# Kernel optimization log

Measured on AMD Instinct MI355X. Metric: run time of the kernel, lower is better.

Reference implementation:

```python
import jax, jax.numpy as jnp
import numpy as np

N0, N1, N2 = 262144, 65536, 16384   # sampled src nodes, layer-1 targets, layer-2 targets
E1, E2 = 1048576, 262144            # fanout 16 edges per layer
IN_C, HID_C, OUT_C = 128, 256, 64


def sage_conv(x_src, x_dst, src, dst, num_dst, W_l, W_r, b):
    # PyG SAGEConv (mean aggr): out = mean_{j in N(i)} x_src[j] @ W_l^T + b + x_dst @ W_r^T
    msgs = x_src[src]                                   # [E, C] gather
    s = jax.ops.segment_sum(msgs, dst, num_segments=num_dst)
    cnt = jax.ops.segment_sum(jnp.ones((src.shape[0],), x_src.dtype), dst,
                              num_segments=num_dst)
    aggr = s / jnp.maximum(cnt, 1.0)[:, None]           # mean; isolated nodes -> 0
    return aggr @ W_l.T + b + x_dst @ W_r.T


def setup_inputs() -> dict:
    key = jax.random.key(0)
    ks = jax.random.split(key, 9)
    inp = {
        "x": jax.random.normal(ks[0], (N0, IN_C), dtype=jnp.float32),
        "src1": jax.random.randint(ks[1], (E1,), 0, N0, dtype=jnp.int32),
        "dst1": jax.random.randint(ks[2], (E1,), 0, N1, dtype=jnp.int32),
        "src2": jax.random.randint(ks[3], (E2,), 0, N1, dtype=jnp.int32),
        "dst2": jax.random.randint(ks[4], (E2,), 0, N2, dtype=jnp.int32),
        "W1_l": jax.random.normal(ks[5], (HID_C, IN_C), dtype=jnp.float32) * 0.05,
        "W1_r": jax.random.normal(ks[6], (HID_C, IN_C), dtype=jnp.float32) * 0.05,
        "b1": jnp.zeros((HID_C,), dtype=jnp.float32),
        "W2_l": jax.random.normal(ks[7], (OUT_C, HID_C), dtype=jnp.float32) * 0.05,
        "W2_r": jax.random.normal(ks[8], (OUT_C, HID_C), dtype=jnp.float32) * 0.05,
        "b2": jnp.zeros((OUT_C,), dtype=jnp.float32),
    }
    return inp


def reference(x, src1, dst1, src2, dst2, W1_l, W1_r, b1, W2_l, W2_r, b2):
    # layer 1: sources = all N0 nodes, targets = first N1 nodes (x_target = x[:size[1]])
    h = sage_conv(x, x[:N1], src1, dst1, N1, W1_l, W1_r, b1)   # [N1, HID_C]
    h = jax.nn.relu(h)   # dropout is identity in eval mode
    # layer 2: sources = N1 layer-1 outputs, targets = first N2
    h = sage_conv(h, h[:N2], src2, dst2, N2, W2_l, W2_r, b2)   # [N2, OUT_C]
    return jax.nn.log_softmax(h, axis=-1)
```

## Files before the change

kernel.cpp:

```cpp
#include <hip/hip_runtime.h>
#include <cstdint>
#include <cstddef>

#define N0C 262144
#define N1C 65536
#define N2C 16384
#define E1C 1048576
#define E2C 262144
#define XN4 (N0C * 128 / 4)
#define XHALF (XN4 / 2)

typedef __attribute__((ext_vector_type(8))) short bf16x8;
typedef __attribute__((ext_vector_type(4))) float f32x4;

__device__ __forceinline__ unsigned short f2bf(float f) {
  union { float f; unsigned u; } q; q.f = f;
  unsigned r = q.u + 0x7fffu + ((q.u >> 16) & 1u);
  return (unsigned short)(r >> 16);
}
__device__ __forceinline__ float blo(unsigned u) {
  union { unsigned u; float f; } q; q.u = u << 16; return q.f;
}
__device__ __forceinline__ float bhi(unsigned u) {
  union { unsigned u; float f; } q; q.u = u & 0xffff0000u; return q.f;
}
__device__ __forceinline__ void gl_lds16(const void* g, void* l) {
  __builtin_amdgcn_global_load_lds((const __attribute__((address_space(1))) void*)g,
                                   (__attribute__((address_space(3))) void*)l, 16, 0, 0);
}

__device__ __forceinline__ void cvt_range(const float4* __restrict__ x,
                                          ushort4* __restrict__ xb,
                                          int i, int stride, int end) {
  for (; i < end; i += stride) {
    float4 v = x[i];
    ushort4 o;
    o.x = f2bf(v.x); o.y = f2bf(v.y); o.z = f2bf(v.z); o.w = f2bf(v.w);
    xb[i] = o;
  }
}

__global__ __launch_bounds__(256) void cvtw_kernel(
    const float4* __restrict__ W1l, const float4* __restrict__ W1r,
    const float4* __restrict__ W2l, const float4* __restrict__ W2r,
    ushort4* __restrict__ W1lb, ushort4* __restrict__ W1rb,
    ushort4* __restrict__ W2lb, ushort4* __restrict__ W2rb,
    int* __restrict__ btail) {
  int y = blockIdx.y;
  int i = blockIdx.x * 256 + threadIdx.x;
  if (y == 4) {
    if (i < 512) btail[i] = 0;
    return;
  }
  const float4* in; ushort4* outp; int n4;
  if (y == 0)      { in = W1l; outp = W1lb; n4 = 8192; }
  else if (y == 1) { in = W1r; outp = W1rb; n4 = 8192; }
  else if (y == 2) { in = W2l; outp = W2lb; n4 = 4096; }
  else             { in = W2r; outp = W2rb; n4 = 4096; }
  if (i < n4) {
    float4 v = in[i];
    ushort4 o;
    o.x = f2bf(v.x); o.y = f2bf(v.y); o.z = f2bf(v.z); o.w = f2bf(v.w);
    outp[i] = o;
  }
}

__global__ __launch_bounds__(256) void mega_kernel(
    const int* __restrict__ src1, const int* __restrict__ dst1,
    const int* __restrict__ src2, const int* __restrict__ dst2,
    int* __restrict__ btail, unsigned* __restrict__ pair1, unsigned* __restrict__ pair2,
    const float4* __restrict__ x, ushort4* __restrict__ xb) {
  __shared__ int hist[256];
  __shared__ int lofs[256];
  __shared__ int gbase[256];
  __shared__ unsigned stg[4096];
  __shared__ unsigned char bstg[4096];
  int b = blockIdx.x;
  int t = threadIdx.x;
  if (b >= 320) {
    cvt_range(x, xb, (b - 320) * 256 + t, 2048 * 256, XHALF);
    return;
  }
  const int* src; const int* dst; int shift; int dmask; int* bt; unsigned* pb; int e0;
  if (b < 256) { src = src1; dst = dst1; shift = 8; dmask = 255; bt = btail;       pb = pair1; e0 = b * 4096; }
  else         { src = src2; dst = dst2; shift = 6; dmask = 63;  bt = btail + 256; pb = pair2; e0 = (b - 256) * 4096; }
  hist[t] = 0;
  __syncthreads();
  unsigned pk[16]; int bk[16], rk[16];
#pragma unroll
  for (int k = 0; k < 16; ++k) {
    int e = e0 + k * 256 + t;
    int s = src[e];
    int d = dst[e];
    bk[k] = d >> shift;
    pk[k] = ((unsigned)(d & dmask) << 18) | (unsigned)s;
    rk[k] = atomicAdd(&hist[bk[k]], 1);
  }
  __syncthreads();
  int v = hist[t];
  lofs[t] = v;
  __syncthreads();
  for (int ofs = 1; ofs < 256; ofs <<= 1) {
    int add = (t >= ofs) ? lofs[t - ofs] : 0;
    __syncthreads();
    lofs[t] += add;
    __syncthreads();
  }
  gbase[t] = atomicAdd(&bt[t], v);
  int excl = lofs[t] - v;
  lofs[t] = excl;
  __syncthreads();
#pragma unroll
  for (int k = 0; k < 16; ++k) {
    int p = lofs[bk[k]] + rk[k];
    stg[p] = pk[k];
    bstg[p] = (unsigned char)bk[k];
  }
  __syncthreads();
  for (int i = t; i < 4096; i += 256) {
    int bki = bstg[i];
    int idx = gbase[bki] + (i - lofs[bki]);
    if (idx < 8192)
      pb[(size_t)bki * 8192 + idx] = stg[i];
  }
}

__global__ __launch_bounds__(256) void binB_kernel(
    const unsigned* __restrict__ pair1, const unsigned* __restrict__ pair2,
    const int* __restrict__ btail,
    int* __restrict__ off1, int* __restrict__ cnt1, int* __restrict__ ssrc1,
    int* __restrict__ off2, int* __restrict__ cnt2, int* __restrict__ ssrc2,
    const float4* __restrict__ x, ushort4* __restrict__ xb) {
  __shared__ int lcnt[256];
  __shared__ int loff[256];
  __shared__ int lcnt2[256];
  __shared__ unsigned stage[8192];
  int b = blockIdx.x;
  int t = threadIdx.x;
  if (b >= 512) {
    cvt_range(x, xb, XHALF + (b - 512) * 256 + t, 2048 * 256, XN4);
    return;
  }
  const unsigned* pb; const int* bt; int dpb; int* off; int* cnt; int* ssrc; int bl;
  if (b < 256) { bl = b;       pb = pair1 + (size_t)bl * 8192; bt = btail;       dpb = 256; off = off1; cnt = cnt1; ssrc = ssrc1; }
  else         { bl = b - 256; pb = pair2 + (size_t)bl * 8192; bt = btail + 256; dpb = 64;  off = off2; cnt = cnt2; ssrc = ssrc2; }
  lcnt[t] = (t < bl) ? bt[t] : 0;
  __syncthreads();
  for (int ofs = 128; ofs > 0; ofs >>= 1) {
    if (t < ofs) lcnt[t] += lcnt[t + ofs];
    __syncthreads();
  }
  int base = lcnt[0];
  __syncthreads();
  lcnt[t] = 0;
  lcnt2[t] = 0;
  __syncthreads();
  int n = bt[bl];
  if (n > 8192) n = 8192;
  for (int i = t; i < n; i += 256) {
    unsigned p = pb[i];
    atomicAdd(&lcnt[p >> 18], 1);
  }
  __syncthreads();
  int v = lcnt[t];
  loff[t] = v;
  __syncthreads();
  for (int ofs = 1; ofs < 256; ofs <<= 1) {
    int add = (t >= ofs) ? loff[t - ofs] : 0;
    __syncthreads();
    loff[t] += add;
    __syncthreads();
  }
  int excl = loff[t] - v;
  loff[t] = excl;
  if (t < dpb) {
    cnt[bl * dpb + t] = v;
    off[bl * dpb + t] = base + excl;
  }
  __syncthreads();
  for (int i = t; i < n; i += 256) {
    unsigned p = pb[i];
    int dl = p >> 18;
    int r = atomicAdd(&lcnt2[dl], 1);
    stage[loff[dl] + r] = p & 0x3FFFFu;
  }
  __syncthreads();
  for (int i = t; i < n; i += 256) ssrc[base + i] = (int)stage[i];
}

__global__ __launch_bounds__(256) void agg1_kernel(const ushort* __restrict__ xb,
                                                   const int* __restrict__ ssrc,
                                                   const int* __restrict__ off,
                                                   const int* __restrict__ cnt,
                                                   ushort* __restrict__ aggr) {
  int wid = (blockIdx.x * 256 + threadIdx.x) >> 6;
  int lane = threadIdx.x & 63;
  int grp = lane >> 4;
  int cl = lane & 15;
  int start = __builtin_amdgcn_readfirstlane(off[wid]);
  int n = __builtin_amdgcn_readfirstlane(cnt[wid]);
  float a0 = 0.f, a1 = 0.f, a2 = 0.f, a3 = 0.f, a4 = 0.f, a5 = 0.f, a6 = 0.f, a7 = 0.f;
  int j = 0;
  for (; j + 8 <= n; j += 8) {
    int sa = ssrc[start + j + grp];
    int sb = ssrc[start + j + 4 + grp];
    uint4 va = *(const uint4*)(xb + (size_t)sa * 128 + cl * 8);
    uint4 vb = *(const uint4*)(xb + (size_t)sb * 128 + cl * 8);
    a0 += blo(va.x) + blo(vb.x); a1 += bhi(va.x) + bhi(vb.x);
    a2 += blo(va.y) + blo(vb.y); a3 += bhi(va.y) + bhi(vb.y);
    a4 += blo(va.z) + blo(vb.z); a5 += bhi(va.z) + bhi(vb.z);
    a6 += blo(va.w) + blo(vb.w); a7 += bhi(va.w) + bhi(vb.w);
  }
  if (j + 4 <= n) {
    int s = ssrc[start + j + grp];
    uint4 v = *(const uint4*)(xb + (size_t)s * 128 + cl * 8);
    a0 += blo(v.x); a1 += bhi(v.x); a2 += blo(v.y); a3 += bhi(v.y);
    a4 += blo(v.z); a5 += bhi(v.z); a6 += blo(v.w); a7 += bhi(v.w);
    j += 4;
  }
  if (grp < n - j) {
    int s = ssrc[start + j + grp];
    uint4 v = *(const uint4*)(xb + (size_t)s * 128 + cl * 8);
    a0 += blo(v.x); a1 += bhi(v.x); a2 += blo(v.y); a3 += bhi(v.y);
    a4 += blo(v.z); a5 += bhi(v.z); a6 += blo(v.w); a7 += bhi(v.w);
  }
#define RED1(v) v += __shfl_xor(v, 16); v += __shfl_xor(v, 32);
  RED1(a0) RED1(a1) RED1(a2) RED1(a3) RED1(a4) RED1(a5) RED1(a6) RED1(a7)
#undef RED1
  if (lane < 16) {
    float inv = (n > 0) ? 1.0f / (float)n : 0.f;
    uint4 o;
    o.x = (unsigned)f2bf(a0 * inv) | ((unsigned)f2bf(a1 * inv) << 16);
    o.y = (unsigned)f2bf(a2 * inv) | ((unsigned)f2bf(a3 * inv) << 16);
    o.z = (unsigned)f2bf(a4 * inv) | ((unsigned)f2bf(a5 * inv) << 16);
    o.w = (unsigned)f2bf(a6 * inv) | ((unsigned)f2bf(a7 * inv) << 16);
    *(uint4*)(aggr + (size_t)wid * 128 + cl * 8) = o;
  }
}

__global__ __launch_bounds__(256) void agg2_kernel(const ushort* __restrict__ h1b,
                                                   const int* __restrict__ ssrc,
                                                   const int* __restrict__ off,
                                                   const int* __restrict__ cnt,
                                                   ushort* __restrict__ aggr) {
  int wid = (blockIdx.x * 256 + threadIdx.x) >> 6;
  int lane = threadIdx.x & 63;
  int grp = lane >> 5;
  int cl = lane & 31;
  int start = __builtin_amdgcn_readfirstlane(off[wid]);
  int n = __builtin_amdgcn_readfirstlane(cnt[wid]);
  float a0 = 0.f, a1 = 0.f, a2 = 0.f, a3 = 0.f, a4 = 0.f, a5 = 0.f, a6 = 0.f, a7 = 0.f;
  int j = 0;
  for (; j + 8 <= n; j += 8) {
    int s0 = ssrc[start + j + grp];
    int s1 = ssrc[start + j + 2 + grp];
    int s2 = ssrc[start + j + 4 + grp];
    int s3 = ssrc[start + j + 6 + grp];
    uint4 v0 = *(const uint4*)(h1b + (size_t)s0 * 256 + cl * 8);
    uint4 v1 = *(const uint4*)(h1b + (size_t)s1 * 256 + cl * 8);
    uint4 v2 = *(const uint4*)(h1b + (size_t)s2 * 256 + cl * 8);
    uint4 v3 = *(const uint4*)(h1b + (size_t)s3 * 256 + cl * 8);
    a0 += blo(v0.x) + blo(v1.x) + blo(v2.x) + blo(v3.x);
    a1 += bhi(v0.x) + bhi(v1.x) + bhi(v2.x) + bhi(v3.x);
    a2 += blo(v0.y) + blo(v1.y) + blo(v2.y) + blo(v3.y);
    a3 += bhi(v0.y) + bhi(v1.y) + bhi(v2.y) + bhi(v3.y);
    a4 += blo(v0.z) + blo(v1.z) + blo(v2.z) + blo(v3.z);
    a5 += bhi(v0.z) + bhi(v1.z) + bhi(v2.z) + bhi(v3.z);
    a6 += blo(v0.w) + blo(v1.w) + blo(v2.w) + blo(v3.w);
    a7 += bhi(v0.w) + bhi(v1.w) + bhi(v2.w) + bhi(v3.w);
  }
  for (; j + 2 <= n; j += 2) {
    int s = ssrc[start + j + grp];
    uint4 v = *(const uint4*)(h1b + (size_t)s * 256 + cl * 8);
    a0 += blo(v.x); a1 += bhi(v.x); a2 += blo(v.y); a3 += bhi(v.y);
    a4 += blo(v.z); a5 += bhi(v.z); a6 += blo(v.w); a7 += bhi(v.w);
  }
  if (grp < n - j) {
    int s = ssrc[start + j + grp];
    uint4 v = *(const uint4*)(h1b + (size_t)s * 256 + cl * 8);
    a0 += blo(v.x); a1 += bhi(v.x); a2 += blo(v.y); a3 += bhi(v.y);
    a4 += blo(v.z); a5 += bhi(v.z); a6 += blo(v.w); a7 += bhi(v.w);
  }
#define RED2(v) v += __shfl_xor(v, 32);
  RED2(a0) RED2(a1) RED2(a2) RED2(a3) RED2(a4) RED2(a5) RED2(a6) RED2(a7)
#undef RED2
  if (lane < 32) {
    float inv = (n > 0) ? 1.0f / (float)n : 0.f;
    uint4 o;
    o.x = (unsigned)f2bf(a0 * inv) | ((unsigned)f2bf(a1 * inv) << 16);
    o.y = (unsigned)f2bf(a2 * inv) | ((unsigned)f2bf(a3 * inv) << 16);
    o.z = (unsigned)f2bf(a4 * inv) | ((unsigned)f2bf(a5 * inv) << 16);
    o.w = (unsigned)f2bf(a6 * inv) | ((unsigned)f2bf(a7 * inv) << 16);
    *(uint4*)(aggr + (size_t)wid * 256 + cl * 8) = o;
  }
}

__global__ __launch_bounds__(512) void mgemm1_kernel(
    const ushort* __restrict__ aggr1, const ushort* __restrict__ xb,
    const ushort* __restrict__ W1lb, const ushort* __restrict__ W1rb,
    const float* __restrict__ b1, ushort* __restrict__ h1b) {
  __shared__ ushort smem[24576];
  ushort* sA = smem;
  ushort* sB = smem + 8192;
  int t = threadIdx.x;
  int lane = t & 63;
  int w = t >> 6;
  int wm = w >> 2, wn = w & 3;
  int i0 = blockIdx.x * 128;

  int sr = t >> 3;
  int sc = (t & 7) ^ (sr & 7);
  int quad = lane >> 4;
  int l15 = lane & 15;
  int xorv = lane & 7;

  f32x4 acc[4][4];
#pragma unroll
  for (int i = 0; i < 4; ++i)
#pragma unroll
    for (int j = 0; j < 4; ++j) acc[i][j] = (f32x4)(0.f);

  for (int kt = 0; kt < 4; ++kt) {
    const ushort* Asrc = (kt < 2) ? aggr1 : xb;
    const ushort* Bsrc = (kt < 2) ? W1lb : W1rb;
    int koff = (kt & 1) * 64;
#pragma unroll
    for (int it = 0; it < 2; ++it) {
      int r = it * 64 + sr;
      gl_lds16(Asrc + (size_t)(i0 + r) * 128 + koff + sc * 8, sA + (it * 512 + t) * 8);
    }
#pragma unroll
    for (int it = 0; it < 4; ++it) {
      int r = it * 64 + sr;
      gl_lds16(Bsrc + (size_t)r * 128 + koff + sc * 8, sB + (it * 512 + t) * 8);
    }
    __syncthreads();
#pragma unroll
    for (int s = 0; s < 2; ++s) {
      int chunk = ((s * 4 + quad) ^ xorv) * 8;
      bf16x8 av[4], bv[4];
#pragma unroll
      for (int fi = 0; fi < 4; ++fi)
        av[fi] = *(const bf16x8*)(sA + (wm * 64 + fi * 16 + l15) * 64 + chunk);
#pragma unroll
      for (int fj = 0; fj < 4; ++fj)
        bv[fj] = *(const bf16x8*)(sB + (wn * 64 + fj * 16 + l15) * 64 + chunk);
#pragma unroll
      for (int fi = 0; fi < 4; ++fi)
#pragma unroll
        for (int fj = 0; fj < 4; ++fj)
          acc[fi][fj] = __builtin_amdgcn_mfma_f32_16x16x32_bf16(av[fi], bv[fj], acc[fi][fj], 0, 0, 0);
    }
    __syncthreads();
  }

  for (int ph = 0; ph < 2; ++ph) {
    if (wm == ph) {
      ushort* eb = smem + (w & 3) * 4096;
#pragma unroll
      for (int fj = 0; fj < 4; ++fj) {
        float bias = b1[wn * 64 + fj * 16 + l15];
#pragma unroll
        for (int fi = 0; fi < 4; ++fi)
#pragma unroll
          for (int r = 0; r < 4; ++r) {
            float v = fmaxf(acc[fi][fj][r] + bias, 0.f);
            eb[(fi * 16 + quad * 4 + r) * 64 + fj * 16 + l15] = f2bf(v);
          }
      }
#pragma unroll
      for (int i = 0; i < 16; ++i) {
        int row = i * 4 + (lane >> 4);
        uint2 v = *(const uint2*)(eb + row * 64 + l15 * 4);
        *(uint2*)(h1b + (size_t)(i0 + wm * 64 + row) * 256 + wn * 64 + l15 * 4) = v;
      }
    }
    __syncthreads();
  }
}

__global__ __launch_bounds__(256) void mgemm2_kernel(
    const ushort* __restrict__ aggr2, const ushort* __restrict__ h1b,
    const ushort* __restrict__ W2lb, const ushort* __restrict__ W2rb,
    const float* __restrict__ b2, float* __restrict__ out) {
  __shared__ ushort sA[64 * 64];
  __shared__ ushort sB[64 * 64];
  int t = threadIdx.x;
  int lane = t & 63;
  int w = t >> 6;
  int i0 = blockIdx.x * 64;

  int sr = t >> 3;
  int sc = (t & 7) ^ (sr & 7);
  int quad = lane >> 4;
  int l15 = lane & 15;
  int xorv = lane & 7;

  f32x4 acc[4];
#pragma unroll
  for (int j = 0; j < 4; ++j) acc[j] = (f32x4)(0.f);

  for (int kt = 0; kt < 8; ++kt) {
    const ushort* Asrc = (kt < 4) ? aggr2 : h1b;
    const ushort* Bsrc = (kt < 4) ? W2lb : W2rb;
    int koff = (kt & 3) * 64;
#pragma unroll
    for (int it = 0; it < 2; ++it) {
      int r = it * 32 + sr;
      gl_lds16(Asrc + (size_t)(i0 + r) * 256 + koff + sc * 8, sA + (it * 256 + t) * 8);
    }
#pragma unroll
    for (int it = 0; it < 2; ++it) {
      int r = it * 32 + sr;
      gl_lds16(Bsrc + (size_t)r * 256 + koff + sc * 8, sB + (it * 256 + t) * 8);
    }
    __syncthreads();
#pragma unroll
    for (int s = 0; s < 2; ++s) {
      int chunk = ((s * 4 + quad) ^ xorv) * 8;
      bf16x8 av = *(const bf16x8*)(sA + (w * 16 + l15) * 64 + chunk);
      bf16x8 bv[4];
#pragma unroll
      for (int fj = 0; fj < 4; ++fj)
        bv[fj] = *(const bf16x8*)(sB + (fj * 16 + l15) * 64 + chunk);
#pragma unroll
      for (int fj = 0; fj < 4; ++fj)
        acc[fj] = __builtin_amdgcn_mfma_f32_16x16x32_bf16(av, bv[fj], acc[fj], 0, 0, 0);
    }
    __syncthreads();
  }

  float b2c[4];
#pragma unroll
  for (int fj = 0; fj < 4; ++fj) b2c[fj] = b2[fj * 16 + l15];

#pragma unroll
  for (int r = 0; r < 4; ++r) {
    int row = i0 + w * 16 + quad * 4 + r;
    float v[4];
#pragma unroll
    for (int fj = 0; fj < 4; ++fj) v[fj] = acc[fj][r] + b2c[fj];
    float m = fmaxf(fmaxf(v[0], v[1]), fmaxf(v[2], v[3]));
    m = fmaxf(m, __shfl_xor(m, 1));
    m = fmaxf(m, __shfl_xor(m, 2));
    m = fmaxf(m, __shfl_xor(m, 4));
    m = fmaxf(m, __shfl_xor(m, 8));
    float ssum = __expf(v[0] - m) + __expf(v[1] - m) + __expf(v[2] - m) + __expf(v[3] - m);
    ssum += __shfl_xor(ssum, 1);
    ssum += __shfl_xor(ssum, 2);
    ssum += __shfl_xor(ssum, 4);
    ssum += __shfl_xor(ssum, 8);
    float lg = m + __logf(ssum);
#pragma unroll
    for (int fj = 0; fj < 4; ++fj)
      out[(size_t)row * 64 + fj * 16 + l15] = v[fj] - lg;
  }
}


extern "C" void kernel_launch(void* const* d_in, const int* in_sizes, int n_in,
                              void* d_out, int out_size, void* d_ws, size_t ws_size,
                              hipStream_t stream) {
  const float* x   = (const float*)d_in[0];
  const int* src1  = (const int*)d_in[1];
  const int* dst1  = (const int*)d_in[2];
  const int* src2  = (const int*)d_in[3];
  const int* dst2  = (const int*)d_in[4];
  const float* W1l = (const float*)d_in[5];
  const float* W1r = (const float*)d_in[6];
  const float* b1  = (const float*)d_in[7];
  const float* W2l = (const float*)d_in[8];
  const float* W2r = (const float*)d_in[9];
  const float* b2  = (const float*)d_in[10];
  float* out = (float*)d_out;

  char* base = (char*)d_ws;
  ushort* xb   = (ushort*)base;
  ushort* ag1b = (ushort*)(base + 67108864);
  ushort* ag2b = (ushort*)(base + 83886080);
  unsigned* pair1 = (unsigned*)(base + 92274688);
  unsigned* pair2 = (unsigned*)(base + 100663296);
  ushort* h1b  = (ushort*)(base + 109051904);
  int* cnt1  = (int*)(base + 142606336);
  int* off1  = cnt1 + N1C;
  int* cnt2  = off1 + N1C;
  int* off2  = cnt2 + N2C;
  int* btail = off2 + N2C;
  int* ssrc1 = btail + 512;
  int* ssrc2 = ssrc1 + E1C;
  ushort* W1lb = (ushort*)(ssrc2 + E2C);
  ushort* W1rb = W1lb + 32768;
  ushort* W2lb = W1rb + 32768;
  ushort* W2rb = W2lb + 16384;

  cvtw_kernel<<<dim3(32, 5), 256, 0, stream>>>(
      (const float4*)W1l, (const float4*)W1r, (const float4*)W2l, (const float4*)W2r,
      (ushort4*)W1lb, (ushort4*)W1rb, (ushort4*)W2lb, (ushort4*)W2rb, btail);

  mega_kernel<<<2368, 256, 0, stream>>>(src1, dst1, src2, dst2, btail, pair1, pair2,
                                        (const float4*)x, (ushort4*)xb);

  binB_kernel<<<2560, 256, 0, stream>>>(pair1, pair2, btail,
                                        off1, cnt1, ssrc1, off2, cnt2, ssrc2,
                                        (const float4*)x, (ushort4*)xb);

  agg1_kernel<<<N1C / 4, 256, 0, stream>>>(xb, ssrc1, off1, cnt1, ag1b);
  mgemm1_kernel<<<N1C / 128, 512, 0, stream>>>(ag1b, xb, W1lb, W1rb, b1, h1b);

  agg2_kernel<<<N2C / 4, 256, 0, stream>>>(h1b, ssrc2, off2, cnt2, ag2b);
  mgemm2_kernel<<<N2C / 64, 256, 0, stream>>>(ag2b, h1b, W2lb, W2rb, b2, out);
}
```

Before: 154.6 us.

## Split layer-1 aggregation and GEMM in halves to overlap them

Layer-1 aggregation and GEMM are split into two row halves. A combined kernel runs the GEMM on the first 32768 rows while its other blocks aggregate the second half, and a final GEMM kernel handles the second half. The aim is to overlap the compute-bound GEMM with the memory-bound gather so the GPU has less idle time between phases. It adds a kernel launch, and because the combined kernel uses 512-thread blocks with a large shared-memory allocation, the aggregation blocks may get lower occupancy.

```diff
diff --git a/kernel.cpp b/kernel.cpp
--- a/kernel.cpp
+++ b/kernel.cpp
@@ -37,6 +37,136 @@
     ushort4 o;
     o.x = f2bf(v.x); o.y = f2bf(v.y); o.z = f2bf(v.z); o.w = f2bf(v.w);
     xb[i] = o;
+  }
+}
+
+__device__ __forceinline__ void agg1_row(const ushort* __restrict__ xb,
+                                         const int* __restrict__ ssrc,
+                                         const int* __restrict__ off,
+                                         const int* __restrict__ cnt,
+                                         ushort* __restrict__ aggr,
+                                         int wid, int lane) {
+  int grp = lane >> 4;
+  int cl = lane & 15;
+  int start = __builtin_amdgcn_readfirstlane(off[wid]);
+  int n = __builtin_amdgcn_readfirstlane(cnt[wid]);
+  float a0 = 0.f, a1 = 0.f, a2 = 0.f, a3 = 0.f, a4 = 0.f, a5 = 0.f, a6 = 0.f, a7 = 0.f;
+  int j = 0;
+  for (; j + 8 <= n; j += 8) {
+    int sa = ssrc[start + j + grp];
+    int sb = ssrc[start + j + 4 + grp];
+    uint4 va = *(const uint4*)(xb + (size_t)sa * 128 + cl * 8);
+    uint4 vb = *(const uint4*)(xb + (size_t)sb * 128 + cl * 8);
+    a0 += blo(va.x) + blo(vb.x); a1 += bhi(va.x) + bhi(vb.x);
+    a2 += blo(va.y) + blo(vb.y); a3 += bhi(va.y) + bhi(vb.y);
+    a4 += blo(va.z) + blo(vb.z); a5 += bhi(va.z) + bhi(vb.z);
+    a6 += blo(va.w) + blo(vb.w); a7 += bhi(va.w) + bhi(vb.w);
+  }
+  if (j + 4 <= n) {
+    int s = ssrc[start + j + grp];
+    uint4 v = *(const uint4*)(xb + (size_t)s * 128 + cl * 8);
+    a0 += blo(v.x); a1 += bhi(v.x); a2 += blo(v.y); a3 += bhi(v.y);
+    a4 += blo(v.z); a5 += bhi(v.z); a6 += blo(v.w); a7 += bhi(v.w);
+    j += 4;
+  }
+  if (grp < n - j) {
+    int s = ssrc[start + j + grp];
+    uint4 v = *(const uint4*)(xb + (size_t)s * 128 + cl * 8);
+    a0 += blo(v.x); a1 += bhi(v.x); a2 += blo(v.y); a3 += bhi(v.y);
+    a4 += blo(v.z); a5 += bhi(v.z); a6 += blo(v.w); a7 += bhi(v.w);
+  }
+#define RED1(v) v += __shfl_xor(v, 16); v += __shfl_xor(v, 32);
+  RED1(a0) RED1(a1) RED1(a2) RED1(a3) RED1(a4) RED1(a5) RED1(a6) RED1(a7)
+#undef RED1
+  if (lane < 16) {
+    float inv = (n > 0) ? 1.0f / (float)n : 0.f;
+    uint4 o;
+    o.x = (unsigned)f2bf(a0 * inv) | ((unsigned)f2bf(a1 * inv) << 16);
+    o.y = (unsigned)f2bf(a2 * inv) | ((unsigned)f2bf(a3 * inv) << 16);
+    o.z = (unsigned)f2bf(a4 * inv) | ((unsigned)f2bf(a5 * inv) << 16);
+    o.w = (unsigned)f2bf(a6 * inv) | ((unsigned)f2bf(a7 * inv) << 16);
+    *(uint4*)(aggr + (size_t)wid * 128 + cl * 8) = o;
+  }
+}
+
+__device__ __forceinline__ void mgemm1_body(
+    const ushort* __restrict__ aggr1, const ushort* __restrict__ xb,
+    const ushort* __restrict__ W1lb, const ushort* __restrict__ W1rb,
+    const float* __restrict__ b1, ushort* __restrict__ h1b,
+    ushort* smem, int i0, int t) {
+  ushort* sA = smem;
+  ushort* sB = smem + 8192;
+  int lane = t & 63;
+  int w = t >> 6;
+  int wm = w >> 2, wn = w & 3;
+  int sr = t >> 3;
+  int sc = (t & 7) ^ (sr & 7);
+  int quad = lane >> 4;
+  int l15 = lane & 15;
+  int xorv = lane & 7;
+
+  f32x4 acc[4][4];
+#pragma unroll
+  for (int i = 0; i < 4; ++i)
+#pragma unroll
+    for (int j = 0; j < 4; ++j) acc[i][j] = (f32x4)(0.f);
+
+  for (int kt = 0; kt < 4; ++kt) {
+    const ushort* Asrc = (kt < 2) ? aggr1 : xb;
+    const ushort* Bsrc = (kt < 2) ? W1lb : W1rb;
+    int koff = (kt & 1) * 64;
+#pragma unroll
+    for (int it = 0; it < 2; ++it) {
+      int r = it * 64 + sr;
+      gl_lds16(Asrc + (size_t)(i0 + r) * 128 + koff + sc * 8, sA + (it * 512 + t) * 8);
+    }
+#pragma unroll
+    for (int it = 0; it < 4; ++it) {
+      int r = it * 64 + sr;
+      gl_lds16(Bsrc + (size_t)r * 128 + koff + sc * 8, sB + (it * 512 + t) * 8);
+    }
+    __syncthreads();
+#pragma unroll
+    for (int s = 0; s < 2; ++s) {
+      int chunk = ((s * 4 + quad) ^ xorv) * 8;
+      bf16x8 av[4], bv[4];
+#pragma unroll
+      for (int fi = 0; fi < 4; ++fi)
+        av[fi] = *(const bf16x8*)(sA + (wm * 64 + fi * 16 + l15) * 64 + chunk);
+#pragma unroll
+      for (int fj = 0; fj < 4; ++fj)
+        bv[fj] = *(const bf16x8*)(sB + (wn * 64 + fj * 16 + l15) * 64 + chunk);
+#pragma unroll
+      for (int fi = 0; fi < 4; ++fi)
+#pragma unroll
+        for (int fj = 0; fj < 4; ++fj)
+          acc[fi][fj] = __builtin_amdgcn_mfma_f32_16x16x32_bf16(av[fi], bv[fj], acc[fi][fj], 0, 0, 0);
+    }
+    __syncthreads();
+  }
+
+  for (int ph = 0; ph < 2; ++ph) {
+    if (wm == ph) {
+      ushort* eb = smem + (w & 3) * 4096;
+#pragma unroll
+      for (int fj = 0; fj < 4; ++fj) {
+        float bias = b1[wn * 64 + fj * 16 + l15];
+#pragma unroll
+        for (int fi = 0; fi < 4; ++fi)
+#pragma unroll
+          for (int r = 0; r < 4; ++r) {
+            float v = fmaxf(acc[fi][fj][r] + bias, 0.f);
+            eb[(fi * 16 + quad * 4 + r) * 64 + fj * 16 + l15] = f2bf(v);
+          }
+      }
+#pragma unroll
+      for (int i = 0; i < 16; ++i) {
+        int row = i * 4 + (lane >> 4);
+        uint2 v = *(const uint2*)(eb + row * 64 + l15 * 4);
+        *(uint2*)(h1b + (size_t)(i0 + wm * 64 + row) * 256 + wn * 64 + l15 * 4) = v;
+      }
+    }
+    __syncthreads();
   }
 }
 
@@ -192,50 +322,35 @@
                                                    const int* __restrict__ ssrc,
                                                    const int* __restrict__ off,
                                                    const int* __restrict__ cnt,
-                                                   ushort* __restrict__ aggr) {
-  int wid = (blockIdx.x * 256 + threadIdx.x) >> 6;
-  int lane = threadIdx.x & 63;
-  int grp = lane >> 4;
-  int cl = lane & 15;
-  int start = __builtin_amdgcn_readfirstlane(off[wid]);
-  int n = __builtin_amdgcn_readfirstlane(cnt[wid]);
-  float a0 = 0.f, a1 = 0.f, a2 = 0.f, a3 = 0.f, a4 = 0.f, a5 = 0.f, a6 = 0.f, a7 = 0.f;
-  int j = 0;
-  for (; j + 8 <= n; j += 8) {
-    int sa = ssrc[start + j + grp];
-    int sb = ssrc[start + j + 4 + grp];
-    uint4 va = *(const uint4*)(xb + (size_t)sa * 128 + cl * 8);
-    uint4 vb = *(const uint4*)(xb + (size_t)sb * 128 + cl * 8);
-    a0 += blo(va.x) + blo(vb.x); a1 += bhi(va.x) + bhi(vb.x);
-    a2 += blo(va.y) + blo(vb.y); a3 += bhi(va.y) + bhi(vb.y);
-    a4 += blo(va.z) + blo(vb.z); a5 += bhi(va.z) + bhi(vb.z);
-    a6 += blo(va.w) + blo(vb.w); a7 += bhi(va.w) + bhi(vb.w);
-  }
-  if (j + 4 <= n) {
-    int s = ssrc[start + j + grp];
-    uint4 v = *(const uint4*)(xb + (size_t)s * 128 + cl * 8);
-    a0 += blo(v.x); a1 += bhi(v.x); a2 += blo(v.y); a3 += bhi(v.y);
-    a4 += blo(v.z); a5 += bhi(v.z); a6 += blo(v.w); a7 += bhi(v.w);
-    j += 4;
-  }
-  if (grp < n - j) {
-    int s = ssrc[start + j + grp];
-    uint4 v = *(const uint4*)(xb + (size_t)s * 128 + cl * 8);
-    a0 += blo(v.x); a1 += bhi(v.x); a2 += blo(v.y); a3 += bhi(v.y);
-    a4 += blo(v.z); a5 += bhi(v.z); a6 += blo(v.w); a7 += bhi(v.w);
-  }
-#define RED1(v) v += __shfl_xor(v, 16); v += __shfl_xor(v, 32);
-  RED1(a0) RED1(a1) RED1(a2) RED1(a3) RED1(a4) RED1(a5) RED1(a6) RED1(a7)
-#undef RED1
-  if (lane < 16) {
-    float inv = (n > 0) ? 1.0f / (float)n : 0.f;
-    uint4 o;
-    o.x = (unsigned)f2bf(a0 * inv) | ((unsigned)f2bf(a1 * inv) << 16);
-    o.y = (unsigned)f2bf(a2 * inv) | ((unsigned)f2bf(a3 * inv) << 16);
-    o.z = (unsigned)f2bf(a4 * inv) | ((unsigned)f2bf(a5 * inv) << 16);
-    o.w = (unsigned)f2bf(a6 * inv) | ((unsigned)f2bf(a7 * inv) << 16);
-    *(uint4*)(aggr + (size_t)wid * 128 + cl * 8) = o;
-  }
+                                                   ushort* __restrict__ aggr,
+                                                   int rbase) {
+  int wid = rbase + ((blockIdx.x * 256 + threadIdx.x) >> 6);
+  agg1_row(xb, ssrc, off, cnt, aggr, wid, threadIdx.x & 63);
+}
+
+__global__ __launch_bounds__(512) void mm1agg_kernel(
+    const ushort* __restrict__ aggr1, const ushort* __restrict__ xb,
+    const ushort* __restrict__ W1lb, const ushort* __restrict__ W1rb,
+    const float* __restrict__ b1, ushort* __restrict__ h1b,
+    const int* __restrict__ ssrc, const int* __restrict__ off,
+    const int* __restrict__ cnt, ushort* __restrict__ aggr_out) {
+  __shared__ ushort smem[24576];
+  int b = blockIdx.x;
+  int t = threadIdx.x;
+  if (b < 256) {
+    mgemm1_body(aggr1, xb, W1lb, W1rb, b1, h1b, smem, b * 128, t);
+  } else {
+    int wid = 32768 + (b - 256) * 8 + (t >> 6);
+    agg1_row(xb, ssrc, off, cnt, aggr_out, wid, t & 63);
+  }
+}
+
+__global__ __launch_bounds__(512) void mgemm1_kernel(
+    const ushort* __restrict__ aggr1, const ushort* __restrict__ xb,
+    const ushort* __restrict__ W1lb, const ushort* __restrict__ W1rb,
+    const float* __restrict__ b1, ushort* __restrict__ h1b, int rbase) {
+  __shared__ ushort smem[24576];
+  mgemm1_body(aggr1, xb, W1lb, W1rb, b1, h1b, smem, rbase + blockIdx.x * 128, threadIdx.x);
 }
 
 __global__ __launch_bounds__(256) void agg2_kernel(const ushort* __restrict__ h1b,
@@ -295,90 +410,6 @@
   }
 }
 
-__global__ __launch_bounds__(512) void mgemm1_kernel(
-    const ushort* __restrict__ aggr1, const ushort* __restrict__ xb,
-    const ushort* __restrict__ W1lb, const ushort* __restrict__ W1rb,
-    const float* __restrict__ b1, ushort* __restrict__ h1b) {
-  __shared__ ushort smem[24576];
-  ushort* sA = smem;
-  ushort* sB = smem + 8192;
-  int t = threadIdx.x;
-  int lane = t & 63;
-  int w = t >> 6;
-  int wm = w >> 2, wn = w & 3;
-  int i0 = blockIdx.x * 128;
-
-  int sr = t >> 3;
-  int sc = (t & 7) ^ (sr & 7);
-  int quad = lane >> 4;
-  int l15 = lane & 15;
-  int xorv = lane & 7;
-
-  f32x4 acc[4][4];
-#pragma unroll
-  for (int i = 0; i < 4; ++i)
-#pragma unroll
-    for (int j = 0; j < 4; ++j) acc[i][j] = (f32x4)(0.f);
-
-  for (int kt = 0; kt < 4; ++kt) {
-    const ushort* Asrc = (kt < 2) ? aggr1 : xb;
-    const ushort* Bsrc = (kt < 2) ? W1lb : W1rb;
-    int koff = (kt & 1) * 64;
-#pragma unroll
-    for (int it = 0; it < 2; ++it) {
-      int r = it * 64 + sr;
-      gl_lds16(Asrc + (size_t)(i0 + r) * 128 + koff + sc * 8, sA + (it * 512 + t) * 8);
-    }
-#pragma unroll
-    for (int it = 0; it < 4; ++it) {
-      int r = it * 64 + sr;
-      gl_lds16(Bsrc + (size_t)r * 128 + koff + sc * 8, sB + (it * 512 + t) * 8);
-    }
-    __syncthreads();
-#pragma unroll
-    for (int s = 0; s < 2; ++s) {
-      int chunk = ((s * 4 + quad) ^ xorv) * 8;
-      bf16x8 av[4], bv[4];
-#pragma unroll
-      for (int fi = 0; fi < 4; ++fi)
-        av[fi] = *(const bf16x8*)(sA + (wm * 64 + fi * 16 + l15) * 64 + chunk);
-#pragma unroll
-      for (int fj = 0; fj < 4; ++fj)
-        bv[fj] = *(const bf16x8*)(sB + (wn * 64 + fj * 16 + l15) * 64 + chunk);
-#pragma unroll
-      for (int fi = 0; fi < 4; ++fi)
-#pragma unroll
-        for (int fj = 0; fj < 4; ++fj)
-          acc[fi][fj] = __builtin_amdgcn_mfma_f32_16x16x32_bf16(av[fi], bv[fj], acc[fi][fj], 0, 0, 0);
-    }
-    __syncthreads();
-  }
-
-  for (int ph = 0; ph < 2; ++ph) {
-    if (wm == ph) {
-      ushort* eb = smem + (w & 3) * 4096;
-#pragma unroll
-      for (int fj = 0; fj < 4; ++fj) {
-        float bias = b1[wn * 64 + fj * 16 + l15];
-#pragma unroll
-        for (int fi = 0; fi < 4; ++fi)
-#pragma unroll
-          for (int r = 0; r < 4; ++r) {
-            float v = fmaxf(acc[fi][fj][r] + bias, 0.f);
-            eb[(fi * 16 + quad * 4 + r) * 64 + fj * 16 + l15] = f2bf(v);
-          }
-      }
-#pragma unroll
-      for (int i = 0; i < 16; ++i) {
-        int row = i * 4 + (lane >> 4);
-        uint2 v = *(const uint2*)(eb + row * 64 + l15 * 4);
-        *(uint2*)(h1b + (size_t)(i0 + wm * 64 + row) * 256 + wn * 64 + l15 * 4) = v;
-      }
-    }
-    __syncthreads();
-  }
-}
-
 __global__ __launch_bounds__(256) void mgemm2_kernel(
     const ushort* __restrict__ aggr2, const ushort* __restrict__ h1b,
     const ushort* __restrict__ W2lb, const ushort* __restrict__ W2rb,
@@ -504,8 +535,10 @@
                                         off1, cnt1, ssrc1, off2, cnt2, ssrc2,
                                         (const float4*)x, (ushort4*)xb);
 
-  agg1_kernel<<<N1C / 4, 256, 0, stream>>>(xb, ssrc1, off1, cnt1, ag1b);
-  mgemm1_kernel<<<N1C / 128, 512, 0, stream>>>(ag1b, xb, W1lb, W1rb, b1, h1b);
+  agg1_kernel<<<8192, 256, 0, stream>>>(xb, ssrc1, off1, cnt1, ag1b, 0);
+  mm1agg_kernel<<<4352, 512, 0, stream>>>(ag1b, xb, W1lb, W1rb, b1, h1b,
+                                          ssrc1, off1, cnt1, ag1b);
+  mgemm1_kernel<<<256, 512, 0, stream>>>(ag1b, xb, W1lb, W1rb, b1, h1b, 32768);
 
   agg2_kernel<<<N2C / 4, 256, 0, stream>>>(h1b, ssrc2, off2, cnt2, ag2b);
   mgemm2_kernel<<<N2C / 64, 256, 0, stream>>>(ag2b, h1b, W2lb, W2rb, b2, out);
```

Result: slower. 182.4 us (+18.0%).
